# Performance work log

Measured on AMD Instinct MI355X. Metric: run time of the kernel, lower is better.

Reference implementation:

```python
import jax, jax.numpy as jnp
import numpy as np

D_INP=36; D_MODEL=144; NHEAD=4; NHID=128; NLAYERS=2
MAX_LEN=215; D_STATIC=9; D_PE=16; N_CLASSES=2; B=128
D_OB=D_MODEL//D_INP; GCH=MAX_LEN*D_OB; D_TR=D_MODEL+D_PE; D_FINAL=D_TR+D_INP
_EI=np.stack(np.nonzero(np.ones((D_INP,D_INP),dtype=np.int64)))  # torch.nonzero(ones).T -> all pairs
SRC_N=jnp.asarray(_EI[0]); TGT_N=jnp.asarray(_EI[1]); N_EDGE=_EI.shape[1]


def setup_inputs():
    ks=jax.random.split(jax.random.key(0),40)
    def w(i,shape,s=0.05): return jax.random.normal(ks[i],shape,jnp.float32)*s
    return {
      'src': jax.random.normal(ks[0],(MAX_LEN,B,2*D_INP),jnp.float32),
      'static': jax.random.normal(ks[1],(B,D_STATIC),jnp.float32),
      'times': jax.random.uniform(ks[2],(MAX_LEN,B),jnp.float32)*MAX_LEN,
      'lengths': jax.random.randint(ks[3],(B,),32,MAX_LEN+1),
      'R_u': w(4,(1,D_INP*D_OB)),
      'emb_w': w(5,(D_INP,D_STATIC)), 'emb_b': jnp.zeros(D_INP,jnp.float32),
      'Wv1': w(6,(GCH,GCH),1.0/np.sqrt(GCH)), 'bv1': jnp.zeros(GCH,jnp.float32),
      'Wv2': w(7,(GCH,GCH),1.0/np.sqrt(GCH)), 'bv2': jnp.zeros(GCH,jnp.float32),
      'in_proj_w': w(8,(NLAYERS,3*D_TR,D_TR)), 'in_proj_b': jnp.zeros((NLAYERS,3*D_TR),jnp.float32),
      'out_w': w(9,(NLAYERS,D_TR,D_TR)), 'out_b': jnp.zeros((NLAYERS,D_TR),jnp.float32),
      'lin1_w': w(10,(NLAYERS,NHID,D_TR)), 'lin1_b': jnp.zeros((NLAYERS,NHID),jnp.float32),
      'lin2_w': w(11,(NLAYERS,D_TR,NHID)), 'lin2_b': jnp.zeros((NLAYERS,D_TR),jnp.float32),
      'ln1_s': jnp.ones((NLAYERS,D_TR),jnp.float32), 'ln1_b': jnp.zeros((NLAYERS,D_TR),jnp.float32),
      'ln2_s': jnp.ones((NLAYERS,D_TR),jnp.float32), 'ln2_b': jnp.zeros((NLAYERS,D_TR),jnp.float32),
      'mlp1_w': w(12,(D_FINAL,D_FINAL)), 'mlp1_b': jnp.zeros(D_FINAL,jnp.float32),
      'mlp2_w': w(13,(N_CLASSES,D_FINAL)), 'mlp2_b': jnp.zeros(N_CLASSES,jnp.float32),
    }


def _seg_softmax(wgt, seg, n):
    m=jnp.full((n,),-jnp.inf,wgt.dtype).at[seg].max(wgt)
    e=jnp.exp(wgt-m[seg])
    s=jnp.zeros((n,),wgt.dtype).at[seg].add(e)
    return e/s[seg]


def _ln(x,s,b):
    mu=jnp.mean(x,-1,keepdims=True); v=jnp.var(x,-1,keepdims=True)
    return (x-mu)/jnp.sqrt(v+1e-5)*s+b


def _forward(src, static, times, R_u, emb_w, emb_b, Wv1, bv1, Wv2, bv2, in_proj_w, in_proj_b, out_w, out_b, lin1_w, lin1_b, lin2_w, lin2_b, ln1_s, ln1_b, ln2_s, ln2_b, mlp1_w, mlp1_b, mlp2_w, mlp2_b, lengths):
    T,Bb=src.shape[0],src.shape[1]
    obs=src[:,:,:D_INP]                                  # drop mask half
    h=jax.nn.relu(jnp.repeat(obs,D_OB,axis=-1)*R_u)      # h_u = relu(x_u*R_u), [T,B,144]
    ts=jnp.asarray(MAX_LEN**np.linspace(0,1,D_PE//2),jnp.float32)
    scaled=times[:,:,None]/ts
    pe=jnp.concatenate([jnp.sin(scaled),jnp.cos(scaled)],-1)  # [T,B,16]
    emb=static@emb_w.T+emb_b                             # [B,36]
    # --- Observation_progation x2 (use_beta=False): gather-softmax-scatter per sensor graph ---
    xb=h.transpose(1,0,2).reshape(Bb,T,D_INP,D_OB).transpose(0,2,1,3).reshape(Bb,D_INP,GCH)
    ew=jnp.ones((N_EDGE,),jnp.float32)                   # adj=ones -> edge_weights=1
    gamma=_seg_softmax(ew,TGT_N,D_INP)                   # softmax over edges per target node
    def prop(x_,Wv,bv):
        V=jax.nn.relu(x_@Wv.T+bv)                        # relu(lin_value(x_j))
        msgs=V[:,SRC_N,:]*gamma[None,:,None]             # gather source features per edge
        return jnp.zeros_like(x_).at[:,TGT_N,:].add(msgs)  # scatter-add to targets
    x1=prop(xb,Wv1,bv1)
    x2=prop(x1,Wv2,bv2)                                  # layer2 uses alpha1 = raw edge_weights
    alpha=jnp.broadcast_to(ew[None,:],(Bb,N_EDGE))       # alpha_all.T
    sq=jnp.sum(alpha*alpha,1)
    d2=jnp.maximum(sq[:,None]+sq[None,:]-2.0*(alpha@alpha.T),0.0)
    distance=jnp.mean(jnp.sqrt(d2))
    out=x2.reshape(Bb,D_INP,T,D_OB).transpose(2,0,1,3).reshape(T,Bb,D_INP*D_OB)
    x=jnp.concatenate([out,pe],-1)                       # [T,B,160]
    mask=jnp.arange(T)[None,:]>=lengths[:,None]          # [B,T] True = padded
    hd=D_TR//NHEAD
    for l in range(NLAYERS):                             # torch post-norm TransformerEncoderLayer
        qkv=x@in_proj_w[l].T+in_proj_b[l]
        q,k,v=jnp.split(qkv,3,-1)
        def heads(t): return t.reshape(T,Bb,NHEAD,hd).transpose(1,2,0,3)  # [B,H,T,hd]
        sc=jnp.einsum('bhqd,bhkd->bhqk',heads(q),heads(k))/np.sqrt(hd)
        sc=jnp.where(mask[:,None,None,:],jnp.float32(-1e30),sc)
        o=jnp.einsum('bhqk,bhkd->bhqd',jax.nn.softmax(sc,-1),heads(v))
        o=o.transpose(2,0,1,3).reshape(T,Bb,D_TR)@out_w[l].T+out_b[l]
        x=_ln(x+o,ln1_s[l],ln1_b[l])
        ff=jax.nn.relu(x@lin1_w[l].T+lin1_b[l])@lin2_w[l].T+lin2_b[l]
        x=_ln(x+ff,ln2_s[l],ln2_b[l])
    valid=1.0-mask.T[:,:,None].astype(x.dtype)           # [T,B,1]
    agg=jnp.sum(x*valid,0)/(lengths[:,None].astype(x.dtype)+1.0)
    feat=jnp.concatenate([agg,emb],1)                    # [B,196]
    logits=jax.nn.relu(feat@mlp1_w.T+mlp1_b)@mlp2_w.T+mlp2_b
    return logits,distance


def reference(src, static, times, lengths, R_u, emb_w, emb_b, Wv1, bv1, Wv2, bv2, in_proj_w, in_proj_b, out_w, out_b, lin1_w, lin1_b, lin2_w, lin2_b, ln1_s, ln1_b, ln2_s, ln2_b, mlp1_w, mlp1_b, mlp2_w, mlp2_b):
    return _forward(src, static, times, R_u, emb_w, emb_b, Wv1, bv1, Wv2, bv2, in_proj_w, in_proj_b, out_w, out_b, lin1_w, lin1_b, lin2_w, lin2_b, ln1_s, ln1_b, ln2_s, ln2_b, mlp1_w, mlp1_b, mlp2_w, mlp2_b, lengths)
```

## Files before the change

### kernel.cpp

```cpp
#include <hip/hip_runtime.h>
#include <math.h>

#define T_LEN 215
#define B_N   128
#define DINP  36
#define D_TR  160
#define HD    40
#define D_FIN 196
#define KPG   864

typedef __attribute__((ext_vector_type(8))) short short8v;
typedef __attribute__((ext_vector_type(4))) float f32x4;

__device__ __forceinline__ ushort f2bf(float x) {
  union { float f; unsigned u; } c; c.f = x;
  unsigned r = c.u + 0x7fffu + ((c.u >> 16) & 1u);
  return (ushort)(r >> 16);
}
__device__ __forceinline__ float bf2f(ushort h) {
  union { unsigned u; float f; } c; c.u = ((unsigned)h) << 16;
  return c.f;
}

__global__ __launch_bounds__(256) void k_prep(const float* __restrict__ Wv1,
    const float* __restrict__ Wv2, const float* __restrict__ ipw, const float* __restrict__ ow,
    const float* __restrict__ l1w, const float* __restrict__ l2w,
    ushort* __restrict__ wv1b, ushort* __restrict__ wv2b, ushort* __restrict__ ipwb,
    ushort* __restrict__ owb, ushort* __restrict__ l1wb, ushort* __restrict__ l2wb,
    float* __restrict__ v2acc, float* __restrict__ featacc) {
  int i = blockIdx.x * 256 + threadIdx.x;
  if (i < 746496) { int n = i / KPG, k = i % KPG;
    wv1b[i] = (n < 860 && k < 860) ? f2bf(Wv1[n * 860 + k]) : (ushort)0; return; }
  i -= 746496;
  if (i < 746496) { int n = i / KPG, k = i % KPG;
    wv2b[i] = (n < 860 && k < 860) ? f2bf(Wv2[n * 860 + k]) : (ushort)0; return; }
  i -= 746496;
  if (i < 153600) { ipwb[i] = f2bf(ipw[i]); return; }
  i -= 153600;
  if (i < 51200)  { owb[i] = f2bf(ow[i]); return; }
  i -= 51200;
  if (i < 40960)  { l1wb[i] = f2bf(l1w[i]); return; }
  i -= 40960;
  if (i < 40960)  { l2wb[i] = f2bf(l2w[i]); return; }
  i -= 40960;
  if (i < 110592) { v2acc[i] = 0.f; return; }
  i -= 110592;
  if (i < 25088)  { featacc[i] = 0.f; return; }
}

__global__ __launch_bounds__(256) void k_xb16(const float* __restrict__ src,
    const float* __restrict__ R_u, ushort* __restrict__ xb16) {
  __shared__ float Ss[T_LEN * DINP];
  const int b = blockIdx.x, tid = threadIdx.x;
  for (int i = tid; i < T_LEN * DINP; i += 256) {
    int t = i / DINP, j = i - t * DINP;
    Ss[i] = src[((size_t)t * B_N + b) * 72 + j];
  }
  __syncthreads();
  for (int i = tid; i < DINP * T_LEN; i += 256) {
    int ii = i / T_LEN, t = i - ii * T_LEN;
    float v = Ss[t * DINP + ii];
    float4 r = ((const float4*)R_u)[ii];
    ushort4 o;
    o.x = f2bf(fmaxf(v * r.x, 0.f)); o.y = f2bf(fmaxf(v * r.y, 0.f));
    o.z = f2bf(fmaxf(v * r.z, 0.f)); o.w = f2bf(fmaxf(v * r.w, 0.f));
    ushort* row = xb16 + (size_t)(b * DINP + ii) * KPG;
    *(ushort4*)(row + 4 * t) = o;
    if (t == 0) { ushort4 z = {0, 0, 0, 0}; *(ushort4*)(row + 860) = z; }
  }
}

__global__ __launch_bounds__(256) void k_red_s1(const ushort* __restrict__ V1b, ushort* __restrict__ s1) {
  int idx = blockIdx.x * 256 + threadIdx.x;
  if (idx >= B_N * KPG) return;
  int b = idx / KPG, n = idx % KPG;
  float s = 0.f;
  if (n < 860) {
    #pragma unroll 4
    for (int i = 0; i < DINP; i++) s += bf2f(V1b[((size_t)b * DINP + i) * 860 + n]);
    s *= (1.0f / 36.0f);
  }
  s1[idx] = (n < 860) ? f2bf(s) : (ushort)0;
}

__global__ __launch_bounds__(256) void k_buildx(const float* __restrict__ v2acc,
    const float* __restrict__ bv2, const float* __restrict__ times,
    float* __restrict__ x, ushort* __restrict__ x16) {
  int idx = blockIdx.x * 256 + threadIdx.x;
  if (idx >= T_LEN * B_N * 40) return;
  int c = idx % 40;
  int r = idx / 40;
  int t = r / B_N, b = r % B_N;
  float4 f;
  if (c < 36) {
    float4 a = *(const float4*)&v2acc[(size_t)b * KPG + 4 * t];
    float4 bb = *(const float4*)&bv2[4 * t];
    f.x = fmaxf(a.x + bb.x, 0.f); f.y = fmaxf(a.y + bb.y, 0.f);
    f.z = fmaxf(a.z + bb.z, 0.f); f.w = fmaxf(a.w + bb.w, 0.f);
  } else {
    float tm = times[r];
    int j0 = (c - 36) * 4;
    bool is_sin = j0 < 8;
    int kb = j0 & 7;
    float o[4];
    #pragma unroll
    for (int qq = 0; qq < 4; qq++) {
      float ts = expf((float)(kb + qq) * 0.76723400f);
      float sc = tm / ts;
      o[qq] = is_sin ? sinf(sc) : cosf(sc);
    }
    f.x = o[0]; f.y = o[1]; f.z = o[2]; f.w = o[3];
  }
  ((float4*)(x + (size_t)r * D_TR))[c] = f;
  ushort4 h = {f2bf(f.x), f2bf(f.y), f2bf(f.z), f2bf(f.w)};
  *(ushort4*)(x16 + (size_t)r * D_TR + 4 * c) = h;
}

template <int RELU, int SPLIT, int WMODE>
__global__ __launch_bounds__(256) void gemm_bf16(const ushort* __restrict__ A,
    const ushort* __restrict__ W, const float* __restrict__ bias, void* __restrict__ Cv,
    int KP, int ldc, int ncols, int kts) {
  __shared__ ushort As[128 * 32];
  __shared__ ushort Ws[64 * 32];
  const int tid = threadIdx.x;
  const int wave = tid >> 6, lane = tid & 63;
  const int lr = lane & 15, hi = lane >> 4;
  const int m0 = blockIdx.y * 128, n0 = blockIdx.x * 64;
  const int kt0 = blockIdx.z * kts;

  f32x4 acc[2][4];
  #pragma unroll
  for (int i = 0; i < 2; i++)
    #pragma unroll
    for (int j = 0; j < 4; j++) acc[i][j] = (f32x4){0.f, 0.f, 0.f, 0.f};

  const int ar = tid >> 2, g = tid & 3;
  const size_t abase0 = (size_t)(m0 + ar) * KP;
  const size_t abase1 = (size_t)(m0 + ar + 64) * KP;
  const size_t bbase  = (size_t)(n0 + ar) * KP;
  const int awb0 = ar * 64 + ((g * 16) ^ ((ar & 3) << 4));
  const int awb1 = awb0 + 64 * 64;
  const int bwb  = ar * 64 + ((g * 16) ^ ((ar & 3) << 4));

  const int arow0 = wave * 32 + lr;
  const int arb0 = arow0 * 64 + ((hi * 16) ^ ((arow0 & 3) << 4));
  const int arb1 = (arow0 + 16) * 64 + ((hi * 16) ^ (((arow0 + 16) & 3) << 4));
  int brb[4];
  #pragma unroll
  for (int j = 0; j < 4; j++)
    brb[j] = (j * 16 + lr) * 64 + ((hi * 16) ^ ((lr & 3) << 4));

  for (int kt = 0; kt < kts; ++kt) {
    const int k0 = (kt0 + kt) * 32;
    uint4 va0 = *(const uint4*)(A + abase0 + k0 + g * 8);
    uint4 va1 = *(const uint4*)(A + abase1 + k0 + g * 8);
    uint4 vb  = *(const uint4*)(W + bbase  + k0 + g * 8);
    if (kt) __syncthreads();
    *(uint4*)((char*)As + awb0) = va0;
    *(uint4*)((char*)As + awb1) = va1;
    *(uint4*)((char*)Ws + bwb)  = vb;
    __syncthreads();
    short8v a0 = *(const short8v*)((const char*)As + arb0);
    short8v a1 = *(const short8v*)((const char*)As + arb1);
    short8v bfr[4];
    #pragma unroll
    for (int j = 0; j < 4; j++) bfr[j] = *(const short8v*)((const char*)Ws + brb[j]);
    #pragma unroll
    for (int j = 0; j < 4; j++) {
      acc[0][j] = __builtin_amdgcn_mfma_f32_16x16x32_bf16(a0, bfr[j], acc[0][j], 0, 0, 0);
      acc[1][j] = __builtin_amdgcn_mfma_f32_16x16x32_bf16(a1, bfr[j], acc[1][j], 0, 0, 0);
    }
  }

  #pragma unroll
  for (int i = 0; i < 2; i++) {
    #pragma unroll
    for (int j = 0; j < 4; j++) {
      int col = n0 + j * 16 + lr;
      int row = m0 + wave * 32 + i * 16 + hi * 4;
      if (col < ncols) {
        if (SPLIT) {
          #pragma unroll
          for (int r = 0; r < 4; r++)
            atomicAdd((float*)Cv + (size_t)(row + r) * ldc + col, acc[i][j][r]);
        } else {
          float bb = bias ? bias[col] : 0.f;
          #pragma unroll
          for (int r = 0; r < 4; r++) {
            float xv = acc[i][j][r] + bb;
            if (RELU) xv = fmaxf(xv, 0.f);
            if (WMODE == 0) ((float*)Cv)[(size_t)(row + r) * ldc + col] = xv;
            else            ((ushort*)Cv)[(size_t)(row + r) * ldc + col] = f2bf(xv);
          }
        }
      }
    }
  }
}

__global__ __launch_bounds__(256) void gemm_ln(const ushort* __restrict__ A,
    const ushort* __restrict__ W, const float* __restrict__ bias,
    const float* __restrict__ gam, const float* __restrict__ bet,
    float* __restrict__ x, ushort* __restrict__ x16, int KP, int kts) {
  __shared__ ushort As[64 * 32];
  __shared__ ushort Ws[160 * 32];
  const int tid = threadIdx.x;
  const int wave = tid >> 6, lane = tid & 63;
  const int lr = lane & 15, hi = lane >> 4;
  const int m0 = blockIdx.x * 64;

  f32x4 acc[10];
  #pragma unroll
  for (int j = 0; j < 10; j++) acc[j] = (f32x4){0.f, 0.f, 0.f, 0.f};

  const int ar = tid >> 2, g = tid & 3;
  const size_t abase = (size_t)(m0 + ar) * KP;
  const int awb = ar * 64 + ((g * 16) ^ ((ar & 3) << 4));
  const int wr0 = tid >> 2,        ws0 = tid & 3;
  const int wr1 = (tid + 256) >> 2, ws1 = (tid + 256) & 3;
  const int wr2 = (tid + 512) >> 2, ws2 = (tid + 512) & 3;
  const int wwb0 = wr0 * 64 + ((ws0 * 16) ^ ((wr0 & 3) << 4));
  const int wwb1 = wr1 * 64 + ((ws1 * 16) ^ ((wr1 & 3) << 4));
  const int wwb2 = wr2 * 64 + ((ws2 * 16) ^ ((wr2 & 3) << 4));

  const int arow = wave * 16 + lr;
  const int arb = arow * 64 + ((hi * 16) ^ ((arow & 3) << 4));
  int brb[10];
  #pragma unroll
  for (int j = 0; j < 10; j++)
    brb[j] = (j * 16 + lr) * 64 + ((hi * 16) ^ ((lr & 3) << 4));

  for (int kt = 0; kt < kts; ++kt) {
    const int k0 = kt * 32;
    uint4 va = *(const uint4*)(A + abase + k0 + g * 8);
    uint4 w0 = *(const uint4*)(W + (size_t)wr0 * KP + k0 + ws0 * 8);
    uint4 w1 = *(const uint4*)(W + (size_t)wr1 * KP + k0 + ws1 * 8);
    uint4 w2;
    if (tid < 128) w2 = *(const uint4*)(W + (size_t)wr2 * KP + k0 + ws2 * 8);
    if (kt) __syncthreads();
    *(uint4*)((char*)As + awb) = va;
    *(uint4*)((char*)Ws + wwb0) = w0;
    *(uint4*)((char*)Ws + wwb1) = w1;
    if (tid < 128) *(uint4*)((char*)Ws + wwb2) = w2;
    __syncthreads();
    short8v a0 = *(const short8v*)((const char*)As + arb);
    #pragma unroll
    for (int j = 0; j < 10; j++) {
      short8v bf = *(const short8v*)((const char*)Ws + brb[j]);
      acc[j] = __builtin_amdgcn_mfma_f32_16x16x32_bf16(a0, bf, acc[j], 0, 0, 0);
    }
  }

  const int rb = m0 + wave * 16 + hi * 4;
  float s[4] = {0.f, 0.f, 0.f, 0.f};
  #pragma unroll
  for (int j = 0; j < 10; j++) {
    const int col = j * 16 + lr;
    const float bb = bias[col];
    #pragma unroll
    for (int r = 0; r < 4; r++) {
      float v = acc[j][r] + bb + x[(size_t)(rb + r) * D_TR + col];
      acc[j][r] = v;
      s[r] += v;
    }
  }
  #pragma unroll
  for (int r = 0; r < 4; r++) {
    s[r] += __shfl_xor(s[r], 1, 64);
    s[r] += __shfl_xor(s[r], 2, 64);
    s[r] += __shfl_xor(s[r], 4, 64);
    s[r] += __shfl_xor(s[r], 8, 64);
  }
  float mu[4], q2[4] = {0.f, 0.f, 0.f, 0.f};
  #pragma unroll
  for (int r = 0; r < 4; r++) mu[r] = s[r] * (1.0f / 160.0f);
  #pragma unroll
  for (int j = 0; j < 10; j++)
    #pragma unroll
    for (int r = 0; r < 4; r++) {
      float d = acc[j][r] - mu[r];
      q2[r] += d * d;
    }
  #pragma unroll
  for (int r = 0; r < 4; r++) {
    q2[r] += __shfl_xor(q2[r], 1, 64);
    q2[r] += __shfl_xor(q2[r], 2, 64);
    q2[r] += __shfl_xor(q2[r], 4, 64);
    q2[r] += __shfl_xor(q2[r], 8, 64);
  }
  float rstd[4];
  #pragma unroll
  for (int r = 0; r < 4; r++) rstd[r] = rsqrtf(q2[r] * (1.0f / 160.0f) + 1e-5f);
  #pragma unroll
  for (int j = 0; j < 10; j++) {
    const int col = j * 16 + lr;
    const float gc = gam[col], bc = bet[col];
    #pragma unroll
    for (int r = 0; r < 4; r++) {
      float o = (acc[j][r] - mu[r]) * rstd[r] * gc + bc;
      x[(size_t)(rb + r) * D_TR + col] = o;
      x16[(size_t)(rb + r) * D_TR + col] = f2bf(o);
    }
  }
}

__global__ __launch_bounds__(256) void k_frag(const ushort* __restrict__ qkv,
    const int* __restrict__ lengths, ushort* __restrict__ Qf,
    ushort* __restrict__ Kf, ushort* __restrict__ Vf) {
  __shared__ ushort Vs[T_LEN * 40];
  const int bh = blockIdx.x, b = bh >> 2, h = bh & 3, tid = threadIdx.x;
  int L = lengths[b]; if (L > T_LEN) L = T_LEN;
  const int nt = (L + 15) >> 4, nvt = (L + 31) >> 5;

  for (int i = tid; i < T_LEN * 5; i += 256) {
    int t = i / 5, g = i - t * 5;
    *(uint4*)&Vs[t * 40 + g * 8] =
        *(const uint4*)(qkv + ((size_t)t * B_N + b) * 480 + 320 + h * 40 + g * 8);
  }

  for (int i = tid; i < nt * 160; i += 256) {
    int tile = i / 160, e = i - tile * 160;
    int isK = e >= 80; if (isK) e -= 80;
    int t, d0;
    if (e < 64) { t = tile * 16 + (e & 15); d0 = (e >> 4) * 8; }
    else        { t = tile * 16 + (e - 64); d0 = 32; }
    uint4 v = {0, 0, 0, 0};
    if (t < T_LEN)
      v = *(const uint4*)(qkv + ((size_t)t * B_N + b) * 480 + (isK ? 160 : 0) + h * 40 + d0);
    ushort* dst = (isK ? Kf : Qf) + (((size_t)bh * 14 + tile) * 80 + e) * 8;
    *(uint4*)dst = v;
  }
  __syncthreads();

  for (int i = tid; i < nvt * 192; i += 256) {
    int kt = i / 192, e = i - kt * 192;
    int l = e & 63, ds = e >> 6;
    int lr = l & 15, hi2 = l >> 4;
    int d = ds * 16 + lr, k0 = kt * 32 + hi2 * 8;
    ushort tmp[8];
    #pragma unroll
    for (int e2 = 0; e2 < 8; e2++) {
      int k = k0 + e2;
      tmp[e2] = (d < 40 && k < T_LEN) ? Vs[k * 40 + d] : (ushort)0;
    }
    *(uint4*)(Vf + (((size_t)bh * 7 + kt) * 192 + e) * 8) = *(uint4*)tmp;
  }
}

__global__ __launch_bounds__(64) void k_attn3(const ushort* __restrict__ Qf,
    const ushort* __restrict__ Kf, const ushort* __restrict__ Vf,
    const int* __restrict__ lengths, ushort* __restrict__ o16) {
  __shared__ ushort SP[16 * 232];
  const int bh = blockIdx.x;
  const int b = bh >> 2, h = bh & 3;
  int L = lengths[b]; if (L > T_LEN) L = T_LEN;
  const int q0 = blockIdx.y << 4;
  if (q0 >= L) return;
  const int lane = threadIdx.x;
  const int lr = lane & 15, hi = lane >> 4;
  const int nk16 = (L + 15) >> 4;
  const int nkt  = (L + 31) >> 5;
  const float SC = 0.15811388300841898f;

  const ushort* qb = Qf + ((size_t)bh * 14 + (q0 >> 4)) * 640;
  uint4 qa0u = *(const uint4*)(qb + lane * 8);
  uint4 qa1u = {0, 0, 0, 0};
  if (hi == 0) qa1u = *(const uint4*)(qb + (64 + lr) * 8);
  short8v qa0 = *(short8v*)&qa0u;
  short8v qa1 = *(short8v*)&qa1u;

  f32x4 c[14];
  #pragma unroll
  for (int kt = 0; kt < 14; ++kt) {
    c[kt] = (f32x4){0.f, 0.f, 0.f, 0.f};
    if (kt < nk16) {
      const ushort* kb = Kf + ((size_t)bh * 14 + kt) * 640;
      uint4 kb0u = *(const uint4*)(kb + lane * 8);
      uint4 kb1u = {0, 0, 0, 0};
      if (hi == 0) kb1u = *(const uint4*)(kb + (64 + lr) * 8);
      c[kt] = __builtin_amdgcn_mfma_f32_16x16x32_bf16(qa0, *(short8v*)&kb0u, c[kt], 0, 0, 0);
      c[kt] = __builtin_amdgcn_mfma_f32_16x16x32_bf16(qa1, *(short8v*)&kb1u, c[kt], 0, 0, 0);
    }
  }

  float mx[4] = {-1e30f, -1e30f, -1e30f, -1e30f};
  #pragma unroll
  for (int kt = 0; kt < 14; ++kt) {
    if (kt < nk16) {
      bool valid = (kt * 16 + lr) < L;
      #pragma unroll
      for (int r = 0; r < 4; r++) {
        float v = valid ? c[kt][r] : -1e30f;
        mx[r] = fmaxf(mx[r], v);
      }
    }
  }
  #pragma unroll
  for (int r = 0; r < 4; r++) {
    mx[r] = fmaxf(mx[r], __shfl_xor(mx[r], 1, 64));
    mx[r] = fmaxf(mx[r], __shfl_xor(mx[r], 2, 64));
    mx[r] = fmaxf(mx[r], __shfl_xor(mx[r], 4, 64));
    mx[r] = fmaxf(mx[r], __shfl_xor(mx[r], 8, 64));
  }
  float sum[4] = {0.f, 0.f, 0.f, 0.f};
  #pragma unroll
  for (int kt = 0; kt < 14; ++kt) {
    if (kt < nk16) {
      bool valid = (kt * 16 + lr) < L;
      #pragma unroll
      for (int r = 0; r < 4; r++) {
        float p = valid ? __expf(SC * (c[kt][r] - mx[r])) : 0.f;
        sum[r] += p;
        c[kt][r] = p;
      }
    }
  }
  #pragma unroll
  for (int r = 0; r < 4; r++) {
    sum[r] += __shfl_xor(sum[r], 1, 64);
    sum[r] += __shfl_xor(sum[r], 2, 64);
    sum[r] += __shfl_xor(sum[r], 4, 64);
    sum[r] += __shfl_xor(sum[r], 8, 64);
  }

  const int nk16w = nkt * 2;
  #pragma unroll
  for (int kt = 0; kt < 14; ++kt) {
    if (kt < nk16w) {
      #pragma unroll
      for (int r = 0; r < 4; r++)
        SP[(hi * 4 + r) * 232 + kt * 16 + lr] = f2bf(c[kt][r]);
    }
  }
  __syncthreads();

  f32x4 o0 = {0.f, 0.f, 0.f, 0.f}, o1 = o0, o2 = o0;
  #pragma unroll
  for (int kt = 0; kt < 7; ++kt) {
    if (kt < nkt) {
      short8v pa = *(const short8v*)((const char*)SP + lr * 464 + kt * 64 + hi * 16);
      const ushort* vb = Vf + ((size_t)bh * 7 + kt) * 1536;
      short8v v0 = *(const short8v*)(vb + lane * 8);
      short8v v1 = *(const short8v*)(vb + 512 + lane * 8);
      short8v v2 = *(const short8v*)(vb + 1024 + lane * 8);
      o0 = __builtin_amdgcn_mfma_f32_16x16x32_bf16(pa, v0, o0, 0, 0, 0);
      o1 = __builtin_amdgcn_mfma_f32_16x16x32_bf16(pa, v1, o1, 0, 0, 0);
      o2 = __builtin_amdgcn_mfma_f32_16x16x32_bf16(pa, v2, o2, 0, 0, 0);
    }
  }

  #pragma unroll
  for (int r = 0; r < 4; r++) {
    int t = q0 + hi * 4 + r;
    if (t < T_LEN) {
      float inv = 1.0f / sum[r];
      ushort* op = o16 + ((size_t)t * B_N + b) * D_TR + h * 40;
      op[lr]      = f2bf(o0[r] * inv);
      op[16 + lr] = f2bf(o1[r] * inv);
      if (lr < 8) op[32 + lr] = f2bf(o2[r] * inv);
    }
  }
}

__global__ __launch_bounds__(256) void k_agg(const float* __restrict__ x,
    const int* __restrict__ lengths, const float* __restrict__ stat,
    const float* __restrict__ emb_w, const float* __restrict__ emb_b,
    float* __restrict__ featacc) {
  const int cx = blockIdx.x, b = blockIdx.y;
  const int tid = threadIdx.x;
  int L = lengths[b]; if (L > T_LEN) L = T_LEN;
  const int c0 = cx * 27;
  if (tid < D_TR) {
    float s = 0.f;
    #pragma unroll
    for (int tl = 0; tl < 27; ++tl) {
      int t = c0 + tl;
      if (t < L) s += x[((size_t)t * B_N + b) * D_TR + tid];
    }
    atomicAdd(&featacc[b * D_FIN + tid], s);
  } else if (cx == 0 && tid < D_FIN) {
    int i = tid - D_TR;
    float s = emb_b[i];
    #pragma unroll
    for (int k = 0; k < 9; k++) s = fmaf(stat[b * 9 + k], emb_w[i * 9 + k], s);
    featacc[b * D_FIN + tid] = s;
  }
}

__global__ __launch_bounds__(256) void k_mlp1(const float* __restrict__ featacc,
    const int* __restrict__ lengths, const float* __restrict__ m1w,
    const float* __restrict__ m1b, float* __restrict__ m1o) {
  const int b = blockIdx.y;
  const int wv = threadIdx.x >> 6, lane = threadIdx.x & 63;
  const int n = blockIdx.x * 4 + wv;
  int L = lengths[b]; if (L > T_LEN) L = T_LEN;
  const float inv = 1.0f / (float)(L + 1);
  const float* wr = m1w + (size_t)n * D_FIN;
  const float* fr = featacc + (size_t)b * D_FIN;
  float s = 0.f;
  for (int k = lane; k < D_FIN; k += 64) {
    float f = fr[k] * (k < D_TR ? inv : 1.f);
    s = fmaf(f, wr[k], s);
  }
  #pragma unroll
  for (int off = 32; off; off >>= 1) s += __shfl_xor(s, off, 64);
  if (lane == 0) m1o[(size_t)b * D_FIN + n] = fmaxf(s + m1b[n], 0.f);
}

__global__ __launch_bounds__(128) void k_logits(const float* __restrict__ m1o,
    const float* __restrict__ m2w, const float* __restrict__ m2b, float* __restrict__ out) {
  const int b = blockIdx.x;
  const int c = threadIdx.x >> 6, lane = threadIdx.x & 63;
  const float* mr = m1o + (size_t)b * D_FIN;
  const float* wr = m2w + c * D_FIN;
  float s = 0.f;
  for (int k = lane; k < D_FIN; k += 64) s = fmaf(mr[k], wr[k], s);
  #pragma unroll
  for (int off = 32; off; off >>= 1) s += __shfl_xor(s, off, 64);
  if (lane == 0) out[2 * b + c] = s + m2b[c];
  if (b == 0 && threadIdx.x == 127) out[256] = 0.f;
}

extern "C" void kernel_launch(void* const* d_in, const int* in_sizes, int n_in,
                              void* d_out, int out_size, void* d_ws, size_t ws_size,
                              hipStream_t stream) {
  const float* src   = (const float*)d_in[0];
  const float* stat  = (const float*)d_in[1];
  const float* times = (const float*)d_in[2];
  const int*   lens  = (const int*)d_in[3];
  const float* R_u   = (const float*)d_in[4];
  const float* emb_w = (const float*)d_in[5];
  const float* emb_b = (const float*)d_in[6];
  const float* Wv1   = (const float*)d_in[7];
  const float* bv1   = (const float*)d_in[8];
  const float* Wv2   = (const float*)d_in[9];
  const float* bv2   = (const float*)d_in[10];
  const float* ipw   = (const float*)d_in[11];
  const float* ipb   = (const float*)d_in[12];
  const float* ow    = (const float*)d_in[13];
  const float* ob    = (const float*)d_in[14];
  const float* l1w   = (const float*)d_in[15];
  const float* l1b   = (const float*)d_in[16];
  const float* l2w   = (const float*)d_in[17];
  const float* l2b   = (const float*)d_in[18];
  const float* ln1s  = (const float*)d_in[19];
  const float* ln1bb = (const float*)d_in[20];
  const float* ln2s  = (const float*)d_in[21];
  const float* ln2bb = (const float*)d_in[22];
  const float* m1w   = (const float*)d_in[23];
  const float* m1b   = (const float*)d_in[24];
  const float* m2w   = (const float*)d_in[25];
  const float* m2b   = (const float*)d_in[26];
  float* out = (float*)d_out;

  char* p = (char*)d_ws;
  float*  x      = (float*)p;   p += 17612800;
  ushort* x16    = (ushort*)p;  p += 8806400;
  float*  v2acc  = (float*)p;   p += 442368;
  ushort* s1b    = (ushort*)p;  p += 221184;
  ushort* obuf16 = (ushort*)p;  p += 8806400;
  ushort* wv1b   = (ushort*)p;  p += 1492992;
  ushort* wv2b   = (ushort*)p;  p += 1492992;
  ushort* ipwb   = (ushort*)p;  p += 307200;
  ushort* owb    = (ushort*)p;  p += 102400;
  ushort* l1wb   = (ushort*)p;  p += 81920;
  ushort* l2wb   = (ushort*)p;  p += 81920;
  float*  featacc= (float*)p;   p += 100352;
  float*  m1o    = (float*)p;   p += 100352;
  char*   R2     = p;
  ushort* xb16   = (ushort*)R2;
  ushort* V1b    = (ushort*)(R2 + 7962624);
  ushort* qkv16  = (ushort*)R2;
  ushort* ffb16  = (ushort*)R2;
  ushort* Qf     = (ushort*)(R2 + 26419200);
  ushort* Kf     = (ushort*)(R2 + 35594240);
  ushort* Vf     = (ushort*)(R2 + 44769280);

  k_prep<<<7482, 256, 0, stream>>>(Wv1, Wv2, ipw, ow, l1w, l2w,
                                   wv1b, wv2b, ipwb, owb, l1wb, l2wb, v2acc, featacc);
  k_xb16<<<128, 256, 0, stream>>>(src, R_u, xb16);

  gemm_bf16<1, 0, 1><<<dim3(14, 36, 1), 256, 0, stream>>>(xb16, wv1b, bv1, V1b, KPG, 860, 860, 27);
  k_red_s1<<<432, 256, 0, stream>>>(V1b, s1b);
  gemm_bf16<0, 1, 0><<<dim3(14, 1, 3), 256, 0, stream>>>(s1b, wv2b, nullptr, v2acc, KPG, KPG, KPG, 9);
  k_buildx<<<4300, 256, 0, stream>>>(v2acc, bv2, times, x, x16);

  for (int l = 0; l < 2; l++) {
    gemm_bf16<0, 0, 1><<<dim3(8, 215, 1), 256, 0, stream>>>(
        x16, ipwb + (size_t)l * 76800, ipb + l * 480, qkv16, 160, 480, 480, 5);
    k_frag<<<512, 256, 0, stream>>>(qkv16, lens, Qf, Kf, Vf);
    k_attn3<<<dim3(512, 14), 64, 0, stream>>>(Qf, Kf, Vf, lens, obuf16);
    gemm_ln<<<430, 256, 0, stream>>>(obuf16, owb + (size_t)l * 25600, ob + l * 160,
                                     ln1s + l * 160, ln1bb + l * 160, x, x16, 160, 5);
    gemm_bf16<1, 0, 1><<<dim3(2, 215, 1), 256, 0, stream>>>(
        x16, l1wb + (size_t)l * 20480, l1b + l * 128, ffb16, 160, 128, 128, 5);
    gemm_ln<<<430, 256, 0, stream>>>(ffb16, l2wb + (size_t)l * 20480, l2b + l * 160,
                                     ln2s + l * 160, ln2bb + l * 160, x, x16, 128, 4);
  }

  k_agg<<<dim3(8, 128), 256, 0, stream>>>(x, lens, stat, emb_w, emb_b, featacc);
  k_mlp1<<<dim3(49, 128), 256, 0, stream>>>(featacc, lens, m1w, m1b, m1o);
  k_logits<<<128, 128, 0, stream>>>(m1o, m2w, m2b, out);
}
```

Measured before the change: 266.7 us.

## Switch activations to batch-major padded layout and drop attention fragment repack kernel

Activations are stored batch-major with the time axis padded to 224 rows, so the attention kernel reads Q and K straight from the QKV GEMM output. The V transpose moves into a new QKV GEMM epilogue that writes a per-head transposed V buffer, which removes the separate k_frag repack kernel and its memory traffic. gemm_bf16 gains an N-tile template parameter (128 for the first graph GEMM), and the split-K factor of the second graph GEMM rises from 3 to 9. In exchange, the padded rows add some wasted work and the attention output's pad rows must be zeroed in prep, and more split-K atomics are issued.

```diff
diff --git a/kernel.cpp b/kernel.cpp
--- a/kernel.cpp
+++ b/kernel.cpp
@@ -2,12 +2,14 @@
 #include <math.h>
 
 #define T_LEN 215
+#define TP    224
 #define B_N   128
 #define DINP  36
 #define D_TR  160
 #define HD    40
 #define D_FIN 196
 #define KPG   864
+#define MROW  28672
 
 typedef __attribute__((ext_vector_type(8))) short short8v;
 typedef __attribute__((ext_vector_type(4))) float f32x4;
@@ -27,7 +29,7 @@
     const float* __restrict__ l1w, const float* __restrict__ l2w,
     ushort* __restrict__ wv1b, ushort* __restrict__ wv2b, ushort* __restrict__ ipwb,
     ushort* __restrict__ owb, ushort* __restrict__ l1wb, ushort* __restrict__ l2wb,
-    float* __restrict__ v2acc, float* __restrict__ featacc) {
+    float* __restrict__ v2acc, float* __restrict__ featacc, ushort* __restrict__ obuf16) {
   int i = blockIdx.x * 256 + threadIdx.x;
   if (i < 746496) { int n = i / KPG, k = i % KPG;
     wv1b[i] = (n < 860 && k < 860) ? f2bf(Wv1[n * 860 + k]) : (ushort)0; return; }
@@ -46,6 +48,12 @@
   if (i < 110592) { v2acc[i] = 0.f; return; }
   i -= 110592;
   if (i < 25088)  { featacc[i] = 0.f; return; }
+  i -= 25088;
+  if (i < 184320) {
+    int b = i / 1440, rem = i % 1440;
+    int t = 215 + rem / 160, cc = rem % 160;
+    obuf16[((size_t)b * TP + t) * D_TR + cc] = 0; return;
+  }
 }
 
 __global__ __launch_bounds__(256) void k_xb16(const float* __restrict__ src,
@@ -87,95 +95,99 @@
     const float* __restrict__ bv2, const float* __restrict__ times,
     float* __restrict__ x, ushort* __restrict__ x16) {
   int idx = blockIdx.x * 256 + threadIdx.x;
-  if (idx >= T_LEN * B_N * 40) return;
+  if (idx >= B_N * TP * 40) return;
   int c = idx % 40;
   int r = idx / 40;
-  int t = r / B_N, b = r % B_N;
-  float4 f;
-  if (c < 36) {
-    float4 a = *(const float4*)&v2acc[(size_t)b * KPG + 4 * t];
-    float4 bb = *(const float4*)&bv2[4 * t];
-    f.x = fmaxf(a.x + bb.x, 0.f); f.y = fmaxf(a.y + bb.y, 0.f);
-    f.z = fmaxf(a.z + bb.z, 0.f); f.w = fmaxf(a.w + bb.w, 0.f);
-  } else {
-    float tm = times[r];
-    int j0 = (c - 36) * 4;
-    bool is_sin = j0 < 8;
-    int kb = j0 & 7;
-    float o[4];
-    #pragma unroll
-    for (int qq = 0; qq < 4; qq++) {
-      float ts = expf((float)(kb + qq) * 0.76723400f);
-      float sc = tm / ts;
-      o[qq] = is_sin ? sinf(sc) : cosf(sc);
-    }
-    f.x = o[0]; f.y = o[1]; f.z = o[2]; f.w = o[3];
+  int t = r % TP, b = r / TP;
+  float4 f = {0.f, 0.f, 0.f, 0.f};
+  if (t < T_LEN) {
+    if (c < 36) {
+      float4 a = *(const float4*)&v2acc[(size_t)b * KPG + 4 * t];
+      float4 bb = *(const float4*)&bv2[4 * t];
+      f.x = fmaxf(a.x + bb.x, 0.f); f.y = fmaxf(a.y + bb.y, 0.f);
+      f.z = fmaxf(a.z + bb.z, 0.f); f.w = fmaxf(a.w + bb.w, 0.f);
+    } else {
+      float tm = times[t * B_N + b];
+      int j0 = (c - 36) * 4;
+      bool is_sin = j0 < 8;
+      int kb = j0 & 7;
+      float o[4];
+      #pragma unroll
+      for (int qq = 0; qq < 4; qq++) {
+        float ts = expf((float)(kb + qq) * 0.76723400f);
+        float sc = tm / ts;
+        o[qq] = is_sin ? sinf(sc) : cosf(sc);
+      }
+      f.x = o[0]; f.y = o[1]; f.z = o[2]; f.w = o[3];
+    }
   }
   ((float4*)(x + (size_t)r * D_TR))[c] = f;
   ushort4 h = {f2bf(f.x), f2bf(f.y), f2bf(f.z), f2bf(f.w)};
   *(ushort4*)(x16 + (size_t)r * D_TR + 4 * c) = h;
 }
 
-template <int RELU, int SPLIT, int WMODE>
+template <int RELU, int SPLIT, int WMODE, int BNT>
 __global__ __launch_bounds__(256) void gemm_bf16(const ushort* __restrict__ A,
     const ushort* __restrict__ W, const float* __restrict__ bias, void* __restrict__ Cv,
     int KP, int ldc, int ncols, int kts) {
   __shared__ ushort As[128 * 32];
-  __shared__ ushort Ws[64 * 32];
+  __shared__ ushort Ws[BNT * 32];
+  constexpr int NJ = BNT / 16;
   const int tid = threadIdx.x;
   const int wave = tid >> 6, lane = tid & 63;
   const int lr = lane & 15, hi = lane >> 4;
-  const int m0 = blockIdx.y * 128, n0 = blockIdx.x * 64;
+  const int m0 = blockIdx.y * 128, n0 = blockIdx.x * BNT;
   const int kt0 = blockIdx.z * kts;
 
-  f32x4 acc[2][4];
+  f32x4 acc[2][NJ];
   #pragma unroll
   for (int i = 0; i < 2; i++)
     #pragma unroll
-    for (int j = 0; j < 4; j++) acc[i][j] = (f32x4){0.f, 0.f, 0.f, 0.f};
+    for (int j = 0; j < NJ; j++) acc[i][j] = (f32x4){0.f, 0.f, 0.f, 0.f};
 
   const int ar = tid >> 2, g = tid & 3;
   const size_t abase0 = (size_t)(m0 + ar) * KP;
   const size_t abase1 = (size_t)(m0 + ar + 64) * KP;
-  const size_t bbase  = (size_t)(n0 + ar) * KP;
+  const size_t bbase0 = (size_t)(n0 + ar) * KP;
+  const size_t bbase1 = (size_t)(n0 + ar + 64) * KP;
   const int awb0 = ar * 64 + ((g * 16) ^ ((ar & 3) << 4));
   const int awb1 = awb0 + 64 * 64;
-  const int bwb  = ar * 64 + ((g * 16) ^ ((ar & 3) << 4));
 
   const int arow0 = wave * 32 + lr;
   const int arb0 = arow0 * 64 + ((hi * 16) ^ ((arow0 & 3) << 4));
   const int arb1 = (arow0 + 16) * 64 + ((hi * 16) ^ (((arow0 + 16) & 3) << 4));
-  int brb[4];
-  #pragma unroll
-  for (int j = 0; j < 4; j++)
+  int brb[NJ];
+  #pragma unroll
+  for (int j = 0; j < NJ; j++)
     brb[j] = (j * 16 + lr) * 64 + ((hi * 16) ^ ((lr & 3) << 4));
 
   for (int kt = 0; kt < kts; ++kt) {
     const int k0 = (kt0 + kt) * 32;
     uint4 va0 = *(const uint4*)(A + abase0 + k0 + g * 8);
     uint4 va1 = *(const uint4*)(A + abase1 + k0 + g * 8);
-    uint4 vb  = *(const uint4*)(W + bbase  + k0 + g * 8);
+    uint4 vb0 = *(const uint4*)(W + bbase0 + k0 + g * 8);
+    uint4 vb1;
+    if constexpr (BNT == 128) vb1 = *(const uint4*)(W + bbase1 + k0 + g * 8);
     if (kt) __syncthreads();
     *(uint4*)((char*)As + awb0) = va0;
     *(uint4*)((char*)As + awb1) = va1;
-    *(uint4*)((char*)Ws + bwb)  = vb;
+    *(uint4*)((char*)Ws + awb0) = vb0;
+    if constexpr (BNT == 128) *(uint4*)((char*)Ws + awb1) = vb1;
     __syncthreads();
     short8v a0 = *(const short8v*)((const char*)As + arb0);
     short8v a1 = *(const short8v*)((const char*)As + arb1);
-    short8v bfr[4];
-    #pragma unroll
-    for (int j = 0; j < 4; j++) bfr[j] = *(const short8v*)((const char*)Ws + brb[j]);
-    #pragma unroll
-    for (int j = 0; j < 4; j++) {
-      acc[0][j] = __builtin_amdgcn_mfma_f32_16x16x32_bf16(a0, bfr[j], acc[0][j], 0, 0, 0);
-      acc[1][j] = __builtin_amdgcn_mfma_f32_16x16x32_bf16(a1, bfr[j], acc[1][j], 0, 0, 0);
+    #pragma unroll
+    for (int j = 0; j < NJ; j++) {
+      short8v bf = *(const short8v*)((const char*)Ws + brb[j]);
+      acc[0][j] = __builtin_amdgcn_mfma_f32_16x16x32_bf16(a0, bf, acc[0][j], 0, 0, 0);
+      acc[1][j] = __builtin_amdgcn_mfma_f32_16x16x32_bf16(a1, bf, acc[1][j], 0, 0, 0);
     }
   }
 
   #pragma unroll
   for (int i = 0; i < 2; i++) {
     #pragma unroll
-    for (int j = 0; j < 4; j++) {
+    for (int j = 0; j < NJ; j++) {
       int col = n0 + j * 16 + lr;
       int row = m0 + wave * 32 + i * 16 + hi * 4;
       if (col < ncols) {
@@ -198,6 +210,86 @@
   }
 }
 
+__global__ __launch_bounds__(256) void gemm_qkv(const ushort* __restrict__ A,
+    const ushort* __restrict__ W, const float* __restrict__ bias,
+    ushort* __restrict__ qkvB, ushort* __restrict__ Vt, int kts) {
+  __shared__ ushort As[128 * 32];
+  __shared__ ushort Ws[128 * 32];
+  const int KP = 160;
+  const int tid = threadIdx.x;
+  const int wave = tid >> 6, lane = tid & 63;
+  const int lr = lane & 15, hi = lane >> 4;
+  const int m0 = blockIdx.y * 128, n0 = blockIdx.x * 128;
+
+  f32x4 acc[2][8];
+  #pragma unroll
+  for (int i = 0; i < 2; i++)
+    #pragma unroll
+    for (int j = 0; j < 8; j++) acc[i][j] = (f32x4){0.f, 0.f, 0.f, 0.f};
+
+  const int ar = tid >> 2, g = tid & 3;
+  const size_t abase0 = (size_t)(m0 + ar) * KP;
+  const size_t abase1 = (size_t)(m0 + ar + 64) * KP;
+  const size_t bbase0 = (size_t)(n0 + ar) * KP;
+  const size_t bbase1 = (size_t)(n0 + ar + 64) * KP;
+  const int awb0 = ar * 64 + ((g * 16) ^ ((ar & 3) << 4));
+  const int awb1 = awb0 + 64 * 64;
+
+  const int arow0 = wave * 32 + lr;
+  const int arb0 = arow0 * 64 + ((hi * 16) ^ ((arow0 & 3) << 4));
+  const int arb1 = (arow0 + 16) * 64 + ((hi * 16) ^ (((arow0 + 16) & 3) << 4));
+  int brb[8];
+  #pragma unroll
+  for (int j = 0; j < 8; j++)
+    brb[j] = (j * 16 + lr) * 64 + ((hi * 16) ^ ((lr & 3) << 4));
+
+  for (int kt = 0; kt < kts; ++kt) {
+    const int k0 = kt * 32;
+    uint4 va0 = *(const uint4*)(A + abase0 + k0 + g * 8);
+    uint4 va1 = *(const uint4*)(A + abase1 + k0 + g * 8);
+    uint4 vb0 = *(const uint4*)(W + bbase0 + k0 + g * 8);
+    uint4 vb1 = *(const uint4*)(W + bbase1 + k0 + g * 8);
+    if (kt) __syncthreads();
+    *(uint4*)((char*)As + awb0) = va0;
+    *(uint4*)((char*)As + awb1) = va1;
+    *(uint4*)((char*)Ws + awb0) = vb0;
+    *(uint4*)((char*)Ws + awb1) = vb1;
+    __syncthreads();
+    short8v a0 = *(const short8v*)((const char*)As + arb0);
+    short8v a1 = *(const short8v*)((const char*)As + arb1);
+    #pragma unroll
+    for (int j = 0; j < 8; j++) {
+      short8v bf = *(const short8v*)((const char*)Ws + brb[j]);
+      acc[0][j] = __builtin_amdgcn_mfma_f32_16x16x32_bf16(a0, bf, acc[0][j], 0, 0, 0);
+      acc[1][j] = __builtin_amdgcn_mfma_f32_16x16x32_bf16(a1, bf, acc[1][j], 0, 0, 0);
+    }
+  }
+
+  #pragma unroll
+  for (int i = 0; i < 2; i++) {
+    const int row = m0 + wave * 32 + i * 16 + hi * 4;
+    const int b = row / TP, t0 = row - b * TP;
+    #pragma unroll
+    for (int j = 0; j < 8; j++) {
+      int col = n0 + j * 16 + lr;
+      if (col < 320) {
+        float bb = bias[col];
+        #pragma unroll
+        for (int r = 0; r < 4; r++)
+          qkvB[(size_t)(row + r) * 480 + col] = f2bf(acc[i][j][r] + bb);
+      } else if (col < 480) {
+        float bb = bias[col];
+        int dg = col - 320;
+        int hh = dg / 40, dd = dg - hh * 40;
+        ushort4 pv;
+        pv.x = f2bf(acc[i][j][0] + bb); pv.y = f2bf(acc[i][j][1] + bb);
+        pv.z = f2bf(acc[i][j][2] + bb); pv.w = f2bf(acc[i][j][3] + bb);
+        *(ushort4*)(Vt + (((size_t)(b * 4 + hh) * 48 + dd) * TP + t0)) = pv;
+      }
+    }
+  }
+}
+
 __global__ __launch_bounds__(256) void gemm_ln(const ushort* __restrict__ A,
     const ushort* __restrict__ W, const float* __restrict__ bias,
     const float* __restrict__ gam, const float* __restrict__ bet,
@@ -216,7 +308,7 @@
   const int ar = tid >> 2, g = tid & 3;
   const size_t abase = (size_t)(m0 + ar) * KP;
   const int awb = ar * 64 + ((g * 16) ^ ((ar & 3) << 4));
-  const int wr0 = tid >> 2,        ws0 = tid & 3;
+  const int wr0 = tid >> 2,         ws0 = tid & 3;
   const int wr1 = (tid + 256) >> 2, ws1 = (tid + 256) & 3;
   const int wr2 = (tid + 512) >> 2, ws2 = (tid + 512) & 3;
   const int wwb0 = wr0 * 64 + ((ws0 * 16) ^ ((wr0 & 3) << 4));
@@ -304,52 +396,9 @@
   }
 }
 
-__global__ __launch_bounds__(256) void k_frag(const ushort* __restrict__ qkv,
-    const int* __restrict__ lengths, ushort* __restrict__ Qf,
-    ushort* __restrict__ Kf, ushort* __restrict__ Vf) {
-  __shared__ ushort Vs[T_LEN * 40];
-  const int bh = blockIdx.x, b = bh >> 2, h = bh & 3, tid = threadIdx.x;
-  int L = lengths[b]; if (L > T_LEN) L = T_LEN;
-  const int nt = (L + 15) >> 4, nvt = (L + 31) >> 5;
-
-  for (int i = tid; i < T_LEN * 5; i += 256) {
-    int t = i / 5, g = i - t * 5;
-    *(uint4*)&Vs[t * 40 + g * 8] =
-        *(const uint4*)(qkv + ((size_t)t * B_N + b) * 480 + 320 + h * 40 + g * 8);
-  }
-
-  for (int i = tid; i < nt * 160; i += 256) {
-    int tile = i / 160, e = i - tile * 160;
-    int isK = e >= 80; if (isK) e -= 80;
-    int t, d0;
-    if (e < 64) { t = tile * 16 + (e & 15); d0 = (e >> 4) * 8; }
-    else        { t = tile * 16 + (e - 64); d0 = 32; }
-    uint4 v = {0, 0, 0, 0};
-    if (t < T_LEN)
-      v = *(const uint4*)(qkv + ((size_t)t * B_N + b) * 480 + (isK ? 160 : 0) + h * 40 + d0);
-    ushort* dst = (isK ? Kf : Qf) + (((size_t)bh * 14 + tile) * 80 + e) * 8;
-    *(uint4*)dst = v;
-  }
-  __syncthreads();
-
-  for (int i = tid; i < nvt * 192; i += 256) {
-    int kt = i / 192, e = i - kt * 192;
-    int l = e & 63, ds = e >> 6;
-    int lr = l & 15, hi2 = l >> 4;
-    int d = ds * 16 + lr, k0 = kt * 32 + hi2 * 8;
-    ushort tmp[8];
-    #pragma unroll
-    for (int e2 = 0; e2 < 8; e2++) {
-      int k = k0 + e2;
-      tmp[e2] = (d < 40 && k < T_LEN) ? Vs[k * 40 + d] : (ushort)0;
-    }
-    *(uint4*)(Vf + (((size_t)bh * 7 + kt) * 192 + e) * 8) = *(uint4*)tmp;
-  }
-}
-
-__global__ __launch_bounds__(64) void k_attn3(const ushort* __restrict__ Qf,
-    const ushort* __restrict__ Kf, const ushort* __restrict__ Vf,
-    const int* __restrict__ lengths, ushort* __restrict__ o16) {
+__global__ __launch_bounds__(64) void k_attn4(const ushort* __restrict__ qkvB,
+    const ushort* __restrict__ Vt, const int* __restrict__ lengths,
+    ushort* __restrict__ o16) {
   __shared__ ushort SP[16 * 232];
   const int bh = blockIdx.x;
   const int b = bh >> 2, h = bh & 3;
@@ -362,10 +411,10 @@
   const int nkt  = (L + 31) >> 5;
   const float SC = 0.15811388300841898f;
 
-  const ushort* qb = Qf + ((size_t)bh * 14 + (q0 >> 4)) * 640;
-  uint4 qa0u = *(const uint4*)(qb + lane * 8);
+  const ushort* qrow = qkvB + ((size_t)b * TP + q0) * 480 + h * 40;
+  uint4 qa0u = *(const uint4*)(qrow + lr * 480 + hi * 8);
   uint4 qa1u = {0, 0, 0, 0};
-  if (hi == 0) qa1u = *(const uint4*)(qb + (64 + lr) * 8);
+  if (hi == 0) qa1u = *(const uint4*)(qrow + lr * 480 + 32);
   short8v qa0 = *(short8v*)&qa0u;
   short8v qa1 = *(short8v*)&qa1u;
 
@@ -374,10 +423,10 @@
   for (int kt = 0; kt < 14; ++kt) {
     c[kt] = (f32x4){0.f, 0.f, 0.f, 0.f};
     if (kt < nk16) {
-      const ushort* kb = Kf + ((size_t)bh * 14 + kt) * 640;
-      uint4 kb0u = *(const uint4*)(kb + lane * 8);
+      const ushort* krow = qkvB + ((size_t)b * TP + kt * 16) * 480 + 160 + h * 40;
+      uint4 kb0u = *(const uint4*)(krow + lr * 480 + hi * 8);
       uint4 kb1u = {0, 0, 0, 0};
-      if (hi == 0) kb1u = *(const uint4*)(kb + (64 + lr) * 8);
+      if (hi == 0) kb1u = *(const uint4*)(krow + lr * 480 + 32);
       c[kt] = __builtin_amdgcn_mfma_f32_16x16x32_bf16(qa0, *(short8v*)&kb0u, c[kt], 0, 0, 0);
       c[kt] = __builtin_amdgcn_mfma_f32_16x16x32_bf16(qa1, *(short8v*)&kb1u, c[kt], 0, 0, 0);
     }
@@ -435,14 +484,15 @@
   __syncthreads();
 
   f32x4 o0 = {0.f, 0.f, 0.f, 0.f}, o1 = o0, o2 = o0;
+  const ushort* vbase = Vt + (size_t)bh * 48 * TP;
   #pragma unroll
   for (int kt = 0; kt < 7; ++kt) {
     if (kt < nkt) {
       short8v pa = *(const short8v*)((const char*)SP + lr * 464 + kt * 64 + hi * 16);
-      const ushort* vb = Vf + ((size_t)bh * 7 + kt) * 1536;
-      short8v v0 = *(const short8v*)(vb + lane * 8);
-      short8v v1 = *(const short8v*)(vb + 512 + lane * 8);
-      short8v v2 = *(const short8v*)(vb + 1024 + lane * 8);
+      const ushort* vb = vbase + kt * 32 + hi * 8;
+      short8v v0 = *(const short8v*)(vb + (size_t)lr * TP);
+      short8v v1 = *(const short8v*)(vb + (size_t)(16 + lr) * TP);
+      short8v v2 = *(const short8v*)(vb + (size_t)(32 + lr) * TP);
       o0 = __builtin_amdgcn_mfma_f32_16x16x32_bf16(pa, v0, o0, 0, 0, 0);
       o1 = __builtin_amdgcn_mfma_f32_16x16x32_bf16(pa, v1, o1, 0, 0, 0);
       o2 = __builtin_amdgcn_mfma_f32_16x16x32_bf16(pa, v2, o2, 0, 0, 0);
@@ -454,7 +504,7 @@
     int t = q0 + hi * 4 + r;
     if (t < T_LEN) {
       float inv = 1.0f / sum[r];
-      ushort* op = o16 + ((size_t)t * B_N + b) * D_TR + h * 40;
+      ushort* op = o16 + ((size_t)b * TP + t) * D_TR + h * 40;
       op[lr]      = f2bf(o0[r] * inv);
       op[16 + lr] = f2bf(o1[r] * inv);
       if (lr < 8) op[32 + lr] = f2bf(o2[r] * inv);
@@ -475,7 +525,7 @@
     #pragma unroll
     for (int tl = 0; tl < 27; ++tl) {
       int t = c0 + tl;
-      if (t < L) s += x[((size_t)t * B_N + b) * D_TR + tid];
+      if (t < L) s += x[((size_t)b * TP + t) * D_TR + tid];
     }
     atomicAdd(&featacc[b * D_FIN + tid], s);
   } else if (cx == 0 && tid < D_FIN) {
@@ -554,11 +604,11 @@
   float* out = (float*)d_out;
 
   char* p = (char*)d_ws;
-  float*  x      = (float*)p;   p += 17612800;
-  ushort* x16    = (ushort*)p;  p += 8806400;
+  float*  x      = (float*)p;   p += 18350080;
+  ushort* x16    = (ushort*)p;  p += 9175040;
   float*  v2acc  = (float*)p;   p += 442368;
   ushort* s1b    = (ushort*)p;  p += 221184;
-  ushort* obuf16 = (ushort*)p;  p += 8806400;
+  ushort* obuf16 = (ushort*)p;  p += 9175040;
   ushort* wv1b   = (ushort*)p;  p += 1492992;
   ushort* wv2b   = (ushort*)p;  p += 1492992;
   ushort* ipwb   = (ushort*)p;  p += 307200;
@@ -570,31 +620,30 @@
   char*   R2     = p;
   ushort* xb16   = (ushort*)R2;
   ushort* V1b    = (ushort*)(R2 + 7962624);
-  ushort* qkv16  = (ushort*)R2;
+  ushort* qkvB   = (ushort*)R2;
   ushort* ffb16  = (ushort*)R2;
-  ushort* Qf     = (ushort*)(R2 + 26419200);
-  ushort* Kf     = (ushort*)(R2 + 35594240);
-  ushort* Vf     = (ushort*)(R2 + 44769280);
-
-  k_prep<<<7482, 256, 0, stream>>>(Wv1, Wv2, ipw, ow, l1w, l2w,
-                                   wv1b, wv2b, ipwb, owb, l1wb, l2wb, v2acc, featacc);
+  ushort* Vt     = (ushort*)(R2 + 27525120);
+
+  k_prep<<<8202, 256, 0, stream>>>(Wv1, Wv2, ipw, ow, l1w, l2w,
+                                   wv1b, wv2b, ipwb, owb, l1wb, l2wb, v2acc, featacc, obuf16);
   k_xb16<<<128, 256, 0, stream>>>(src, R_u, xb16);
 
-  gemm_bf16<1, 0, 1><<<dim3(14, 36, 1), 256, 0, stream>>>(xb16, wv1b, bv1, V1b, KPG, 860, 860, 27);
+  gemm_bf16<1, 0, 1, 128><<<dim3(7, 36, 1), 256, 0, stream>>>(
+      xb16, wv1b, bv1, V1b, KPG, 860, 860, 27);
   k_red_s1<<<432, 256, 0, stream>>>(V1b, s1b);
-  gemm_bf16<0, 1, 0><<<dim3(14, 1, 3), 256, 0, stream>>>(s1b, wv2b, nullptr, v2acc, KPG, KPG, KPG, 9);
-  k_buildx<<<4300, 256, 0, stream>>>(v2acc, bv2, times, x, x16);
+  gemm_bf16<0, 1, 0, 64><<<dim3(14, 1, 9), 256, 0, stream>>>(
+      s1b, wv2b, nullptr, v2acc, KPG, KPG, KPG, 3);
+  k_buildx<<<4480, 256, 0, stream>>>(v2acc, bv2, times, x, x16);
 
   for (int l = 0; l < 2; l++) {
-    gemm_bf16<0, 0, 1><<<dim3(8, 215, 1), 256, 0, stream>>>(
-        x16, ipwb + (size_t)l * 76800, ipb + l * 480, qkv16, 160, 480, 480, 5);
-    k_frag<<<512, 256, 0, stream>>>(qkv16, lens, Qf, Kf, Vf);
-    k_attn3<<<dim3(512, 14), 64, 0, stream>>>(Qf, Kf, Vf, lens, obuf16);
-    gemm_ln<<<430, 256, 0, stream>>>(obuf16, owb + (size_t)l * 25600, ob + l * 160,
+    gemm_qkv<<<dim3(4, 224, 1), 256, 0, stream>>>(
+        x16, ipwb + (size_t)l * 76800, ipb + l * 480, qkvB, Vt, 5);
+    k_attn4<<<dim3(512, 14), 64, 0, stream>>>(qkvB, Vt, lens, obuf16);
+    gemm_ln<<<448, 256, 0, stream>>>(obuf16, owb + (size_t)l * 25600, ob + l * 160,
                                      ln1s + l * 160, ln1bb + l * 160, x, x16, 160, 5);
-    gemm_bf16<1, 0, 1><<<dim3(2, 215, 1), 256, 0, stream>>>(
+    gemm_bf16<1, 0, 1, 64><<<dim3(2, 224, 1), 256, 0, stream>>>(
         x16, l1wb + (size_t)l * 20480, l1b + l * 128, ffb16, 160, 128, 128, 5);
-    gemm_ln<<<430, 256, 0, stream>>>(ffb16, l2wb + (size_t)l * 20480, l2b + l * 160,
+    gemm_ln<<<448, 256, 0, stream>>>(ffb16, l2wb + (size_t)l * 20480, l2b + l * 160,
                                      ln2s + l * 160, ln2bb + l * 160, x, x16, 128, 4);
   }
 
```

Result: faster. 254.1 us (-4.7%).
